# Kernel tuning notes

Hardware: AMD Instinct MI355X
Metric: run time of the kernel (lower is better)

Reference implementation:

```python
import jax, jax.numpy as jnp
import numpy as np


def _lstm_scan(x, w_ih, w_hh, b_ih, b_hh):
    """Unidirectional LSTM, PyTorch gate order (i, f, g, o).
    x: [B, T, C]; w_ih: [4H, C]; w_hh: [4H, H]. Returns [B, T, H]."""
    H = w_hh.shape[1]
    # Precompute input contribution for all timesteps (one big GEMM).
    xg = jnp.einsum('btc,gc->btg', x, w_ih) + b_ih + b_hh  # [B, T, 4H]

    def step(carry, xg_t):
        h, c = carry
        gates = xg_t + h @ w_hh.T
        i, f, g, o = jnp.split(gates, 4, axis=-1)
        c = jax.nn.sigmoid(f) * c + jax.nn.sigmoid(i) * jnp.tanh(g)
        h = jax.nn.sigmoid(o) * jnp.tanh(c)
        return (h, c), h

    B = x.shape[0]
    h0 = jnp.zeros((B, H), x.dtype)
    _, hs = jax.lax.scan(step, (h0, h0), jnp.swapaxes(xg, 0, 1))
    return jnp.swapaxes(hs, 0, 1)  # [B, T, H]


def _bilstm(x, w_ih_f, w_hh_f, b_ih_f, b_hh_f, w_ih_b, w_hh_b, b_ih_b, b_hh_b):
    fwd = _lstm_scan(x, w_ih_f, w_hh_f, b_ih_f, b_hh_f)
    bwd = _lstm_scan(x[:, ::-1], w_ih_b, w_hh_b, b_ih_b, b_hh_b)[:, ::-1]
    return jnp.concatenate([fwd, bwd], axis=-1)  # [B, T, 2H]


def setup_inputs() -> dict:
    key = jax.random.key(0)
    B, Hh, Ww, C, Hd = 64, 48, 48, 192, 48
    ks = jax.random.split(key, 20)
    s = 1.0 / np.sqrt(Hd)  # PyTorch LSTM init scale
    inp = {"x": jax.random.normal(ks[0], (B, Hh, Ww, C), jnp.float32)}
    names = ["v_w_ih_f", "v_w_hh_f", "v_b_ih_f", "v_b_hh_f",
             "v_w_ih_b", "v_w_hh_b", "v_b_ih_b", "v_b_hh_b",
             "h_w_ih_f", "h_w_hh_f", "h_b_ih_f", "h_b_hh_f",
             "h_w_ih_b", "h_w_hh_b", "h_b_ih_b", "h_b_hh_b"]
    shapes = [(4 * Hd, C), (4 * Hd, Hd), (4 * Hd,), (4 * Hd,)] * 4
    for i, (n, sh) in enumerate(zip(names, shapes)):
        inp[n] = jax.random.uniform(ks[1 + i], sh, jnp.float32, -s, s)
    inp["proj_w"] = jax.random.uniform(ks[17], (C, 4 * Hd), jnp.float32, -s, s)
    inp["proj_b"] = jax.random.uniform(ks[18], (C,), jnp.float32, -s, s)
    return inp


def reference(x, v_w_ih_f, v_w_hh_f, v_b_ih_f, v_b_hh_f,
              v_w_ih_b, v_w_hh_b, v_b_ih_b, v_b_hh_b,
              h_w_ih_f, h_w_hh_f, h_b_ih_f, h_b_hh_f,
              h_w_ih_b, h_w_hh_b, h_b_ih_b, h_b_hh_b,
              proj_w, proj_b):
    B, Hh, Ww, C = x.shape
    # Vertical: scan over height for each column.
    xv = jnp.transpose(x, (0, 2, 1, 3)).reshape(B * Ww, Hh, C)
    v = _bilstm(xv, v_w_ih_f, v_w_hh_f, v_b_ih_f, v_b_hh_f,
                v_w_ih_b, v_w_hh_b, v_b_ih_b, v_b_hh_b)
    v = jnp.transpose(v.reshape(B, Ww, Hh, -1), (0, 2, 1, 3))  # [B,H,W,2Hd]
    # Horizontal: scan over width for each row.
    xh = x.reshape(B * Hh, Ww, C)
    h = _bilstm(xh, h_w_ih_f, h_w_hh_f, h_b_ih_f, h_b_hh_f,
                h_w_ih_b, h_w_hh_b, h_b_ih_b, h_b_hh_b)
    h = h.reshape(B, Hh, Ww, -1)  # [B,H,W,2Hd]
    combined = jnp.concatenate([v, h], axis=-1)  # [B,H,W,4Hd]
    return jnp.einsum('bhwk,ck->bhwc', combined, proj_w) + proj_b
```

## Files before the change

kernel.cpp:

```cpp
#include <hip/hip_runtime.h>

typedef short short8 __attribute__((ext_vector_type(8)));
typedef short short4v __attribute__((ext_vector_type(4)));
typedef float f32x4 __attribute__((ext_vector_type(4)));
typedef unsigned short u16;

__device__ __forceinline__ u16 f2bf(float f) {
  unsigned int u = __builtin_bit_cast(unsigned int, f);
  u = (u + 0x7FFFu + ((u >> 16) & 1u)) >> 16;
  return (u16)u;
}
__device__ __forceinline__ short8 cvt8(float4 a, float4 b) {
  short8 v;
  v[0] = (short)f2bf(a.x); v[1] = (short)f2bf(a.y);
  v[2] = (short)f2bf(a.z); v[3] = (short)f2bf(a.w);
  v[4] = (short)f2bf(b.x); v[5] = (short)f2bf(b.y);
  v[6] = (short)f2bf(b.z); v[7] = (short)f2bf(b.w);
  return v;
}
__device__ __forceinline__ float sigmoidf_fast(float x) {
  return __builtin_amdgcn_rcpf(1.0f + __expf(-x));
}
__device__ __forceinline__ float tanhf_fast(float x) {
  return 1.0f - 2.0f * __builtin_amdgcn_rcpf(1.0f + __expf(2.0f * x));
}

#define NPX 147456

__global__ __launch_bounds__(256)
void xcvt_kernel(const float* __restrict__ x, u16* __restrict__ xbf)
{
  size_t c = ((size_t)blockIdx.x * 256 + threadIdx.x) * 8;
  const float4* p = (const float4*)(x + c);
  *(short8*)(xbf + c) = cvt8(p[0], p[1]);
}

__global__ __launch_bounds__(192)
void fused_scan_kernel(const u16* __restrict__ xbf,
    const float* __restrict__ wi0, const float* __restrict__ wi1,
    const float* __restrict__ wi2, const float* __restrict__ wi3,
    const float* __restrict__ u0, const float* __restrict__ u1,
    const float* __restrict__ u2, const float* __restrict__ u3,
    const float* __restrict__ bi0, const float* __restrict__ bh0,
    const float* __restrict__ bi1, const float* __restrict__ bh1,
    const float* __restrict__ bi2, const float* __restrict__ bh2,
    const float* __restrict__ bi3, const float* __restrict__ bh3,
    u16* __restrict__ comb)
{
  __shared__ u16 hl[2][1152];
  const int tid  = threadIdx.x;
  const int lane = tid & 63;
  const int wv   = tid >> 6;
  const int cl   = lane & 15;
  const int kg   = lane >> 4;
  const int W    = blockIdx.x;
  const int dir  = W / 192;
  const int g    = W - dir * 192;
  const int bb   = g / 3;
  const int rc   = (g - bb * 3) * 16 + cl;
  const bool vert = dir < 2;
  const bool bwd  = (dir & 1) != 0;

  const float* wp  = dir == 0 ? wi0 : dir == 1 ? wi1 : dir == 2 ? wi2 : wi3;
  const float* up  = dir == 0 ? u0  : dir == 1 ? u1  : dir == 2 ? u2  : u3;
  const float* bip = dir == 0 ? bi0 : dir == 1 ? bi1 : dir == 2 ? bi2 : bi3;
  const float* bhp = dir == 0 ? bh0 : dir == 1 ? bh1 : dir == 2 ? bh2 : bh3;

  const int tp0 = bwd ? 47 : 0;
  int px = vert ? (bb * 48 + tp0) * 48 + rc : (bb * 48 + rc) * 48 + tp0;
  const int dpx = (vert ? 48 : 1) * (bwd ? -1 : 1);

  short8 xfA[6], xfB[6];
  {
    const u16* xp = xbf + (size_t)px * 192 + kg * 8;
    #pragma unroll
    for (int kk = 0; kk < 6; ++kk) xfA[kk] = *(const short8*)(xp + kk * 32);
    const u16* xq = xbf + (size_t)(px + dpx) * 192 + kg * 8;
    #pragma unroll
    for (int kk = 0; kk < 6; ++kk) xfB[kk] = *(const short8*)(xq + kk * 32);
  }

  short8 wf[4][6];
  #pragma unroll
  for (int q = 0; q < 4; ++q) {
    int n = q * 48 + wv * 16 + cl;
    #pragma unroll
    for (int kk = 0; kk < 6; ++kk) {
      const float4* p = (const float4*)(wp + n * 192 + kk * 32 + kg * 8);
      wf[q][kk] = cvt8(p[0], p[1]);
    }
  }
  short8 uf[4][2];
  #pragma unroll
  for (int q = 0; q < 4; ++q) {
    int n = q * 48 + wv * 16 + cl;
    {
      const float4* p = (const float4*)(up + n * 48 + kg * 8);
      uf[q][0] = cvt8(p[0], p[1]);
    }
    if (kg < 2) {
      const float4* p = (const float4*)(up + n * 48 + 32 + kg * 8);
      uf[q][1] = cvt8(p[0], p[1]);
    } else {
      short8 z = {}; uf[q][1] = z;
    }
  }
  f32x4 bv[4];
  #pragma unroll
  for (int q = 0; q < 4; ++q)
    #pragma unroll
    for (int r = 0; r < 4; ++r) {
      int n = q * 48 + wv * 16 + kg * 4 + r;
      bv[q][r] = bip[n] + bhp[n];
    }

  u16* hz = &hl[0][0];
  for (int i = tid; i < 2304; i += 192) hz[i] = 0;
  __syncthreads();

  float c[4] = {0.f, 0.f, 0.f, 0.f};
  int cur = 0;
  u16* cb = comb + (size_t)dir * NPX * 48 + wv * 16 + kg * 4;

  const u16* xk = xbf + kg * 8;

  for (int it = 0; it < 24; ++it) {
    #pragma unroll
    for (int half = 0; half < 2; ++half) {
      short8* xf = half ? xfB : xfA;

      f32x4 acc[4];
      #pragma unroll
      for (int q = 0; q < 4; ++q) acc[q] = bv[q];
      #pragma unroll
      for (int kk = 0; kk < 6; ++kk)
        #pragma unroll
        for (int q = 0; q < 4; ++q)
          acc[q] = __builtin_amdgcn_mfma_f32_16x16x32_bf16(wf[q][kk], xf[kk], acc[q], 0, 0, 0);

      {
        int pp = px + 2 * dpx;
        pp = (pp < 0 || pp >= NPX) ? 0 : pp;
        const u16* xp = xk + (size_t)pp * 192;
        #pragma unroll
        for (int kk = 0; kk < 6; ++kk) xf[kk] = *(const short8*)(xp + kk * 32);
      }

      short8 hb0 = *(const short8*)&hl[cur][cl * 72 + kg * 8];
      short8 hb1 = *(const short8*)&hl[cur][cl * 72 + 32 + kg * 8];
      #pragma unroll
      for (int q = 0; q < 4; ++q)
        acc[q] = __builtin_amdgcn_mfma_f32_16x16x32_bf16(uf[q][0], hb0, acc[q], 0, 0, 0);
      #pragma unroll
      for (int q = 0; q < 4; ++q)
        acc[q] = __builtin_amdgcn_mfma_f32_16x16x32_bf16(uf[q][1], hb1, acc[q], 0, 0, 0);

      short4v h4;
      #pragma unroll
      for (int r = 0; r < 4; ++r) {
        float ii = sigmoidf_fast(acc[0][r]);
        float ff = sigmoidf_fast(acc[1][r]);
        float gg = tanhf_fast(acc[2][r]);
        float oo = sigmoidf_fast(acc[3][r]);
        float cc = ff * c[r] + ii * gg;
        c[r] = cc;
        h4[r] = (short)f2bf(oo * tanhf_fast(cc));
      }
      *(short4v*)&hl[cur ^ 1][cl * 72 + wv * 16 + kg * 4] = h4;
      *(short4v*)(cb + (size_t)px * 48) = h4;
      __syncthreads();
      cur ^= 1;
      px += dpx;
    }
  }
}

__global__ __launch_bounds__(256)
void proj_kernel(const u16* __restrict__ comb,
                 const float* __restrict__ pw,
                 const float* __restrict__ pb,
                 float* __restrict__ out)
{
  __shared__ u16 al[12288];
  const int tid  = threadIdx.x;
  const int lane = tid & 63;
  const int wv   = tid >> 6;
  const int cl   = lane & 15;
  const int kg   = lane >> 4;
  const int pxb  = blockIdx.x * 64;

  #pragma unroll
  for (int i = 0; i < 6; ++i) {
    int ch = tid + 256 * i;
    int pxl = ch / 24;
    int k0  = (ch % 24) << 3;
    int d   = k0 / 48;
    short8 v = *(const short8*)(comb + ((size_t)d * NPX + pxb + pxl) * 48 + (k0 - d * 48));
    *(short8*)&al[(pxl * 192 + k0) ^ ((pxl & 7) << 3)] = v;
  }

  short8 wf[3][6];
  #pragma unroll
  for (int nt = 0; nt < 3; ++nt) {
    int n = wv * 48 + nt * 16 + cl;
    #pragma unroll
    for (int kk = 0; kk < 6; ++kk) {
      const float4* p = (const float4*)(pw + n * 192 + kk * 32 + kg * 8);
      wf[nt][kk] = cvt8(p[0], p[1]);
    }
  }
  f32x4 bv[3];
  #pragma unroll
  for (int nt = 0; nt < 3; ++nt)
    #pragma unroll
    for (int r = 0; r < 4; ++r)
      bv[nt][r] = pb[wv * 48 + nt * 16 + kg * 4 + r];

  __syncthreads();

  f32x4 acc[3][4];
  #pragma unroll
  for (int nt = 0; nt < 3; ++nt)
    #pragma unroll
    for (int mi = 0; mi < 4; ++mi) acc[nt][mi] = bv[nt];

  #pragma unroll
  for (int kk = 0; kk < 6; ++kk) {
    short8 bfr[4];
    #pragma unroll
    for (int mi = 0; mi < 4; ++mi) {
      int row = mi * 16 + cl;
      bfr[mi] = *(const short8*)&al[(row * 192 + kk * 32 + kg * 8) ^ ((row & 7) << 3)];
    }
    #pragma unroll
    for (int nt = 0; nt < 3; ++nt)
      #pragma unroll
      for (int mi = 0; mi < 4; ++mi)
        acc[nt][mi] = __builtin_amdgcn_mfma_f32_16x16x32_bf16(wf[nt][kk], bfr[mi], acc[nt][mi], 0, 0, 0);
  }

  #pragma unroll
  for (int nt = 0; nt < 3; ++nt)
    #pragma unroll
    for (int mi = 0; mi < 4; ++mi) {
      size_t o = (size_t)(pxb + mi * 16 + cl) * 192 + wv * 48 + nt * 16 + kg * 4;
      *(f32x4*)(out + o) = acc[nt][mi];
    }
}

extern "C" void kernel_launch(void* const* d_in, const int* in_sizes, int n_in,
                              void* d_out, int out_size, void* d_ws, size_t ws_size,
                              hipStream_t stream) {
  const float* x = (const float*)d_in[0];
  u16* xbf  = (u16*)d_ws;
  u16* comb = (u16*)d_ws + (size_t)NPX * 192;

  xcvt_kernel<<<13824, 256, 0, stream>>>(x, xbf);

  fused_scan_kernel<<<768, 192, 0, stream>>>(
      xbf,
      (const float*)d_in[1], (const float*)d_in[5],
      (const float*)d_in[9], (const float*)d_in[13],
      (const float*)d_in[2], (const float*)d_in[6],
      (const float*)d_in[10], (const float*)d_in[14],
      (const float*)d_in[3],  (const float*)d_in[4],
      (const float*)d_in[7],  (const float*)d_in[8],
      (const float*)d_in[11], (const float*)d_in[12],
      (const float*)d_in[15], (const float*)d_in[16],
      comb);

  proj_kernel<<<2304, 256, 0, stream>>>(
      comb, (const float*)d_in[17], (const float*)d_in[18], (float*)d_out);
}
```

Measured before the change: 217.6 us.

## Split LSTM gate GEMMs across twice the waves and stage x through LDS

The scan kernel now launches 384 threads per block. Each wave pair splits the four gates: one wave computes i/f and the other g/o, and the g/o accumulators are exchanged through shared memory so that one wave applies the nonlinearities. The x tile for the next timestep is loaded cooperatively into a swizzled, double-buffered LDS buffer instead of per-lane register prefetch. The weights are prescaled by log2(e) so the activations can use exp2 directly. This halves the MFMA chain per wave on the serial critical path. In exchange it adds an extra barrier per step, LDS traffic, and half the waves sit idle during the activation phase.

```diff
diff --git a/kernel.cpp b/kernel.cpp
--- a/kernel.cpp
+++ b/kernel.cpp
@@ -18,14 +18,17 @@
   v[6] = (short)f2bf(b.z); v[7] = (short)f2bf(b.w);
   return v;
 }
-__device__ __forceinline__ float sigmoidf_fast(float x) {
-  return __builtin_amdgcn_rcpf(1.0f + __expf(-x));
-}
-__device__ __forceinline__ float tanhf_fast(float x) {
-  return 1.0f - 2.0f * __builtin_amdgcn_rcpf(1.0f + __expf(2.0f * x));
+__device__ __forceinline__ short8 cvt8s(float4 a, float4 b, float s) {
+  short8 v;
+  v[0] = (short)f2bf(a.x * s); v[1] = (short)f2bf(a.y * s);
+  v[2] = (short)f2bf(a.z * s); v[3] = (short)f2bf(a.w * s);
+  v[4] = (short)f2bf(b.x * s); v[5] = (short)f2bf(b.y * s);
+  v[6] = (short)f2bf(b.z * s); v[7] = (short)f2bf(b.w * s);
+  return v;
 }
 
 #define NPX 147456
+#define L2E 1.44269504088896f
 
 __global__ __launch_bounds__(256)
 void xcvt_kernel(const float* __restrict__ x, u16* __restrict__ xbf)
@@ -35,7 +38,7 @@
   *(short8*)(xbf + c) = cvt8(p[0], p[1]);
 }
 
-__global__ __launch_bounds__(192)
+__global__ __launch_bounds__(384)
 void fused_scan_kernel(const u16* __restrict__ xbf,
     const float* __restrict__ wi0, const float* __restrict__ wi1,
     const float* __restrict__ wi2, const float* __restrict__ wi3,
@@ -47,17 +50,23 @@
     const float* __restrict__ bi3, const float* __restrict__ bh3,
     u16* __restrict__ comb)
 {
+  __shared__ u16 xl[2][3072];
   __shared__ u16 hl[2][1152];
+  __shared__ f32x4 xga[3][64];
+  __shared__ f32x4 xgo[3][64];
+
   const int tid  = threadIdx.x;
   const int lane = tid & 63;
   const int wv   = tid >> 6;
+  const int s    = wv >> 1;
+  const int h    = wv & 1;
   const int cl   = lane & 15;
   const int kg   = lane >> 4;
   const int W    = blockIdx.x;
   const int dir  = W / 192;
   const int g    = W - dir * 192;
   const int bb   = g / 3;
-  const int rc   = (g - bb * 3) * 16 + cl;
+  const int rcb  = (g - bb * 3) * 16;
   const bool vert = dir < 2;
   const bool bwd  = (dir & 1) != 0;
 
@@ -67,111 +76,113 @@
   const float* bhp = dir == 0 ? bh0 : dir == 1 ? bh1 : dir == 2 ? bh2 : bh3;
 
   const int tp0 = bwd ? 47 : 0;
-  int px = vert ? (bb * 48 + tp0) * 48 + rc : (bb * 48 + rc) * 48 + tp0;
   const int dpx = (vert ? 48 : 1) * (bwd ? -1 : 1);
 
-  short8 xfA[6], xfB[6];
-  {
-    const u16* xp = xbf + (size_t)px * 192 + kg * 8;
-    #pragma unroll
-    for (int kk = 0; kk < 6; ++kk) xfA[kk] = *(const short8*)(xp + kk * 32);
-    const u16* xq = xbf + (size_t)(px + dpx) * 192 + kg * 8;
-    #pragma unroll
-    for (int kk = 0; kk < 6; ++kk) xfB[kk] = *(const short8*)(xq + kk * 32);
-  }
-
-  short8 wf[4][6];
-  #pragma unroll
-  for (int q = 0; q < 4; ++q) {
-    int n = q * 48 + wv * 16 + cl;
+  const int seq_l = tid / 24;
+  const int k0    = (tid % 24) * 8;
+  const int rc_t  = rcb + seq_l;
+  const int px_t0 = vert ? (bb * 48 + tp0) * 48 + rc_t
+                         : (bb * 48 + rc_t) * 48 + tp0;
+  const int swz_w = (seq_l * 192 + k0) ^ ((seq_l & 7) << 3);
+
+  short8 s0 = *(const short8*)(xbf + (size_t)px_t0 * 192 + k0);
+  *(short8*)&xl[0][swz_w] = s0;
+  const u16* xsrc = xbf + (size_t)(px_t0 + dpx) * 192 + k0;
+  const ptrdiff_t xstep = (ptrdiff_t)dpx * 192;
+
+  const int g0 = h ? 2 : 0;
+  const int g1 = h ? 3 : 1;
+  const float s0f = h ? 2.0f * L2E : L2E;
+  const float s1f = L2E;
+
+  short8 wf[2][6], uf[2][2];
+  f32x4 bv[2];
+  #pragma unroll
+  for (int j = 0; j < 2; ++j) {
+    int gj = j ? g1 : g0;
+    float sc = j ? s1f : s0f;
+    int n = gj * 48 + s * 16 + cl;
     #pragma unroll
     for (int kk = 0; kk < 6; ++kk) {
       const float4* p = (const float4*)(wp + n * 192 + kk * 32 + kg * 8);
-      wf[q][kk] = cvt8(p[0], p[1]);
-    }
-  }
-  short8 uf[4][2];
-  #pragma unroll
-  for (int q = 0; q < 4; ++q) {
-    int n = q * 48 + wv * 16 + cl;
+      wf[j][kk] = cvt8s(p[0], p[1], sc);
+    }
     {
       const float4* p = (const float4*)(up + n * 48 + kg * 8);
-      uf[q][0] = cvt8(p[0], p[1]);
+      uf[j][0] = cvt8s(p[0], p[1], sc);
     }
     if (kg < 2) {
       const float4* p = (const float4*)(up + n * 48 + 32 + kg * 8);
-      uf[q][1] = cvt8(p[0], p[1]);
+      uf[j][1] = cvt8s(p[0], p[1], sc);
     } else {
-      short8 z = {}; uf[q][1] = z;
-    }
-  }
-  f32x4 bv[4];
-  #pragma unroll
-  for (int q = 0; q < 4; ++q)
+      short8 z = {}; uf[j][1] = z;
+    }
     #pragma unroll
     for (int r = 0; r < 4; ++r) {
-      int n = q * 48 + wv * 16 + kg * 4 + r;
-      bv[q][r] = bip[n] + bhp[n];
-    }
-
-  u16* hz = &hl[0][0];
-  for (int i = tid; i < 2304; i += 192) hz[i] = 0;
+      int nb = gj * 48 + s * 16 + kg * 4 + r;
+      bv[j][r] = (bip[nb] + bhp[nb]) * sc;
+    }
+  }
+
+  for (int i = tid; i < 2304; i += 384) (&hl[0][0])[i] = 0;
   __syncthreads();
 
   float c[4] = {0.f, 0.f, 0.f, 0.f};
-  int cur = 0;
-  u16* cb = comb + (size_t)dir * NPX * 48 + wv * 16 + kg * 4;
-
-  const u16* xk = xbf + kg * 8;
-
-  for (int it = 0; it < 24; ++it) {
-    #pragma unroll
-    for (int half = 0; half < 2; ++half) {
-      short8* xf = half ? xfB : xfA;
-
-      f32x4 acc[4];
-      #pragma unroll
-      for (int q = 0; q < 4; ++q) acc[q] = bv[q];
-      #pragma unroll
-      for (int kk = 0; kk < 6; ++kk)
-        #pragma unroll
-        for (int q = 0; q < 4; ++q)
-          acc[q] = __builtin_amdgcn_mfma_f32_16x16x32_bf16(wf[q][kk], xf[kk], acc[q], 0, 0, 0);
-
-      {
-        int pp = px + 2 * dpx;
-        pp = (pp < 0 || pp >= NPX) ? 0 : pp;
-        const u16* xp = xk + (size_t)pp * 192;
-        #pragma unroll
-        for (int kk = 0; kk < 6; ++kk) xf[kk] = *(const short8*)(xp + kk * 32);
-      }
-
-      short8 hb0 = *(const short8*)&hl[cur][cl * 72 + kg * 8];
-      short8 hb1 = *(const short8*)&hl[cur][cl * 72 + 32 + kg * 8];
-      #pragma unroll
-      for (int q = 0; q < 4; ++q)
-        acc[q] = __builtin_amdgcn_mfma_f32_16x16x32_bf16(uf[q][0], hb0, acc[q], 0, 0, 0);
-      #pragma unroll
-      for (int q = 0; q < 4; ++q)
-        acc[q] = __builtin_amdgcn_mfma_f32_16x16x32_bf16(uf[q][1], hb1, acc[q], 0, 0, 0);
-
+  const int rc_l = rcb + cl;
+  const int px_l = vert ? (bb * 48 + tp0) * 48 + rc_l
+                        : (bb * 48 + rc_l) * 48 + tp0;
+  u16* cbp = comb + (size_t)dir * NPX * 48 + (size_t)px_l * 48 + s * 16 + kg * 4;
+  const ptrdiff_t cstep = (ptrdiff_t)dpx * 48;
+
+  int cur = 0, hcur = 0;
+
+  for (int t = 0; t < 48; ++t) {
+    short8 sa;
+    if (t < 47) { sa = *(const short8*)xsrc; xsrc += xstep; }
+
+    short8 xf[6];
+    #pragma unroll
+    for (int kk = 0; kk < 6; ++kk)
+      xf[kk] = *(const short8*)&xl[cur][(cl * 192 + kk * 32 + kg * 8) ^ ((cl & 7) << 3)];
+    short8 hb0 = *(const short8*)&hl[hcur][cl * 72 + kg * 8];
+    short8 hb1 = *(const short8*)&hl[hcur][cl * 72 + 32 + kg * 8];
+
+    f32x4 a0 = bv[0], a1 = bv[1];
+    #pragma unroll
+    for (int kk = 0; kk < 6; ++kk) {
+      a0 = __builtin_amdgcn_mfma_f32_16x16x32_bf16(wf[0][kk], xf[kk], a0, 0, 0, 0);
+      a1 = __builtin_amdgcn_mfma_f32_16x16x32_bf16(wf[1][kk], xf[kk], a1, 0, 0, 0);
+    }
+    a0 = __builtin_amdgcn_mfma_f32_16x16x32_bf16(uf[0][0], hb0, a0, 0, 0, 0);
+    a1 = __builtin_amdgcn_mfma_f32_16x16x32_bf16(uf[1][0], hb0, a1, 0, 0, 0);
+    a0 = __builtin_amdgcn_mfma_f32_16x16x32_bf16(uf[0][1], hb1, a0, 0, 0, 0);
+    a1 = __builtin_amdgcn_mfma_f32_16x16x32_bf16(uf[1][1], hb1, a1, 0, 0, 0);
+
+    if (h) { xga[s][lane] = a0; xgo[s][lane] = a1; }
+    __syncthreads();
+
+    if (!h) {
+      f32x4 aG = xga[s][lane];
+      f32x4 aO = xgo[s][lane];
       short4v h4;
       #pragma unroll
       for (int r = 0; r < 4; ++r) {
-        float ii = sigmoidf_fast(acc[0][r]);
-        float ff = sigmoidf_fast(acc[1][r]);
-        float gg = tanhf_fast(acc[2][r]);
-        float oo = sigmoidf_fast(acc[3][r]);
+        float ii = __builtin_amdgcn_rcpf(1.0f + __builtin_exp2f(-a0[r]));
+        float ff = __builtin_amdgcn_rcpf(1.0f + __builtin_exp2f(-a1[r]));
+        float gg = 1.0f - 2.0f * __builtin_amdgcn_rcpf(1.0f + __builtin_exp2f(aG[r]));
+        float oo = __builtin_amdgcn_rcpf(1.0f + __builtin_exp2f(-aO[r]));
         float cc = ff * c[r] + ii * gg;
         c[r] = cc;
-        h4[r] = (short)f2bf(oo * tanhf_fast(cc));
+        float th = 1.0f - 2.0f * __builtin_amdgcn_rcpf(1.0f + __builtin_exp2f(cc * (2.0f * L2E)));
+        h4[r] = (short)f2bf(oo * th);
       }
-      *(short4v*)&hl[cur ^ 1][cl * 72 + wv * 16 + kg * 4] = h4;
-      *(short4v*)(cb + (size_t)px * 48) = h4;
-      __syncthreads();
-      cur ^= 1;
-      px += dpx;
-    }
+      *(short4v*)&hl[hcur ^ 1][cl * 72 + s * 16 + kg * 4] = h4;
+      *(short4v*)cbp = h4;
+      cbp += cstep;
+    }
+    if (t < 47) *(short8*)&xl[cur ^ 1][swz_w] = sa;
+    __syncthreads();
+    cur ^= 1; hcur ^= 1;
   }
 }
 
@@ -193,10 +204,10 @@
   for (int i = 0; i < 6; ++i) {
     int ch = tid + 256 * i;
     int pxl = ch / 24;
-    int k0  = (ch % 24) << 3;
-    int d   = k0 / 48;
-    short8 v = *(const short8*)(comb + ((size_t)d * NPX + pxb + pxl) * 48 + (k0 - d * 48));
-    *(short8*)&al[(pxl * 192 + k0) ^ ((pxl & 7) << 3)] = v;
+    int kk0 = (ch % 24) << 3;
+    int d   = kk0 / 48;
+    short8 v = *(const short8*)(comb + ((size_t)d * NPX + pxb + pxl) * 48 + (kk0 - d * 48));
+    *(short8*)&al[(pxl * 192 + kk0) ^ ((pxl & 7) << 3)] = v;
   }
 
   short8 wf[3][6];
@@ -209,12 +220,12 @@
       wf[nt][kk] = cvt8(p[0], p[1]);
     }
   }
-  f32x4 bv[3];
+  f32x4 bvv[3];
   #pragma unroll
   for (int nt = 0; nt < 3; ++nt)
     #pragma unroll
     for (int r = 0; r < 4; ++r)
-      bv[nt][r] = pb[wv * 48 + nt * 16 + kg * 4 + r];
+      bvv[nt][r] = pb[wv * 48 + nt * 16 + kg * 4 + r];
 
   __syncthreads();
 
@@ -222,7 +233,7 @@
   #pragma unroll
   for (int nt = 0; nt < 3; ++nt)
     #pragma unroll
-    for (int mi = 0; mi < 4; ++mi) acc[nt][mi] = bv[nt];
+    for (int mi = 0; mi < 4; ++mi) acc[nt][mi] = bvv[nt];
 
   #pragma unroll
   for (int kk = 0; kk < 6; ++kk) {
@@ -257,7 +268,7 @@
 
   xcvt_kernel<<<13824, 256, 0, stream>>>(x, xbf);
 
-  fused_scan_kernel<<<768, 192, 0, stream>>>(
+  fused_scan_kernel<<<768, 384, 0, stream>>>(
       xbf,
       (const float*)d_in[1], (const float*)d_in[5],
       (const float*)d_in[9], (const float*)d_in[13],
```

After: 312.7 us. 43.7% more time.

## Software-pipeline input-projection MFMAs across steps and fold log2e into weights

Applied to the files above, without the earlier changes.

The scan loop now computes the next timestep's input-gate MFMAs (W_ih·x) before the current step's recurrent MFMAs, using ping-pong accumulators, so the x-dependent matrix work sits off the h-dependent critical path. Weights and biases are pre-scaled by log2(e) (twice that for the g gate), so the sigmoid and tanh can use exp2 directly without a multiply. The x prefetch becomes a single buffer advanced by pointer stride, with no bounds clamping. The trade-off is extra accumulator registers, plus a small rounding change because the scaling is applied before the bf16 conversion.

```diff
diff --git a/kernel.cpp b/kernel.cpp
--- a/kernel.cpp
+++ b/kernel.cpp
@@ -18,14 +18,17 @@
   v[6] = (short)f2bf(b.z); v[7] = (short)f2bf(b.w);
   return v;
 }
-__device__ __forceinline__ float sigmoidf_fast(float x) {
-  return __builtin_amdgcn_rcpf(1.0f + __expf(-x));
-}
-__device__ __forceinline__ float tanhf_fast(float x) {
-  return 1.0f - 2.0f * __builtin_amdgcn_rcpf(1.0f + __expf(2.0f * x));
+__device__ __forceinline__ short8 cvt8s(float4 a, float4 b, float s) {
+  short8 v;
+  v[0] = (short)f2bf(a.x * s); v[1] = (short)f2bf(a.y * s);
+  v[2] = (short)f2bf(a.z * s); v[3] = (short)f2bf(a.w * s);
+  v[4] = (short)f2bf(b.x * s); v[5] = (short)f2bf(b.y * s);
+  v[6] = (short)f2bf(b.z * s); v[7] = (short)f2bf(b.w * s);
+  return v;
 }
 
 #define NPX 147456
+#define L2E 1.44269504088896f
 
 __global__ __launch_bounds__(256)
 void xcvt_kernel(const float* __restrict__ x, u16* __restrict__ xbf)
@@ -67,111 +70,112 @@
   const float* bhp = dir == 0 ? bh0 : dir == 1 ? bh1 : dir == 2 ? bh2 : bh3;
 
   const int tp0 = bwd ? 47 : 0;
-  int px = vert ? (bb * 48 + tp0) * 48 + rc : (bb * 48 + rc) * 48 + tp0;
   const int dpx = (vert ? 48 : 1) * (bwd ? -1 : 1);
-
-  short8 xfA[6], xfB[6];
-  {
-    const u16* xp = xbf + (size_t)px * 192 + kg * 8;
-    #pragma unroll
-    for (int kk = 0; kk < 6; ++kk) xfA[kk] = *(const short8*)(xp + kk * 32);
-    const u16* xq = xbf + (size_t)(px + dpx) * 192 + kg * 8;
-    #pragma unroll
-    for (int kk = 0; kk < 6; ++kk) xfB[kk] = *(const short8*)(xq + kk * 32);
-  }
-
-  short8 wf[4][6];
+  const int px0 = vert ? (bb * 48 + tp0) * 48 + rc : (bb * 48 + rc) * 48 + tp0;
+
+  const u16* xp = xbf + (size_t)px0 * 192 + kg * 8;
+  const ptrdiff_t xstep = (ptrdiff_t)dpx * 192;
+
+  short8 xf[6];
+  #pragma unroll
+  for (int kk = 0; kk < 6; ++kk) xf[kk] = *(const short8*)(xp + kk * 32);
+
+  short8 wf[4][6], uf[4][2];
+  f32x4 bv[4];
   #pragma unroll
   for (int q = 0; q < 4; ++q) {
+    const float sc = (q == 2) ? 2.0f * L2E : L2E;
     int n = q * 48 + wv * 16 + cl;
     #pragma unroll
     for (int kk = 0; kk < 6; ++kk) {
       const float4* p = (const float4*)(wp + n * 192 + kk * 32 + kg * 8);
-      wf[q][kk] = cvt8(p[0], p[1]);
-    }
-  }
-  short8 uf[4][2];
-  #pragma unroll
-  for (int q = 0; q < 4; ++q) {
-    int n = q * 48 + wv * 16 + cl;
+      wf[q][kk] = cvt8s(p[0], p[1], sc);
+    }
     {
       const float4* p = (const float4*)(up + n * 48 + kg * 8);
-      uf[q][0] = cvt8(p[0], p[1]);
+      uf[q][0] = cvt8s(p[0], p[1], sc);
     }
     if (kg < 2) {
       const float4* p = (const float4*)(up + n * 48 + 32 + kg * 8);
-      uf[q][1] = cvt8(p[0], p[1]);
+      uf[q][1] = cvt8s(p[0], p[1], sc);
     } else {
       short8 z = {}; uf[q][1] = z;
     }
-  }
-  f32x4 bv[4];
-  #pragma unroll
-  for (int q = 0; q < 4; ++q)
     #pragma unroll
     for (int r = 0; r < 4; ++r) {
-      int n = q * 48 + wv * 16 + kg * 4 + r;
-      bv[q][r] = bip[n] + bhp[n];
-    }
-
-  u16* hz = &hl[0][0];
-  for (int i = tid; i < 2304; i += 192) hz[i] = 0;
+      int nb = q * 48 + wv * 16 + kg * 4 + r;
+      bv[q][r] = (bip[nb] + bhp[nb]) * sc;
+    }
+  }
+
+  for (int i = tid; i < 2304; i += 192) (&hl[0][0])[i] = 0;
   __syncthreads();
 
+  f32x4 pA[4], pB[4];
+  #pragma unroll
+  for (int q = 0; q < 4; ++q) pA[q] = bv[q];
+  #pragma unroll
+  for (int kk = 0; kk < 6; ++kk)
+    #pragma unroll
+    for (int q = 0; q < 4; ++q)
+      pA[q] = __builtin_amdgcn_mfma_f32_16x16x32_bf16(wf[q][kk], xf[kk], pA[q], 0, 0, 0);
+  xp += xstep;
+  #pragma unroll
+  for (int kk = 0; kk < 6; ++kk) xf[kk] = *(const short8*)(xp + kk * 32);
+
   float c[4] = {0.f, 0.f, 0.f, 0.f};
-  int cur = 0;
-  u16* cb = comb + (size_t)dir * NPX * 48 + wv * 16 + kg * 4;
-
-  const u16* xk = xbf + kg * 8;
-
-  for (int it = 0; it < 24; ++it) {
-    #pragma unroll
-    for (int half = 0; half < 2; ++half) {
-      short8* xf = half ? xfB : xfA;
-
-      f32x4 acc[4];
+  int hcur = 0;
+  u16* cbp = comb + (size_t)dir * NPX * 48 + (size_t)px0 * 48 + wv * 16 + kg * 4;
+  const ptrdiff_t cstep = (ptrdiff_t)dpx * 48;
+
+  auto STEP = [&](f32x4 (&cur)[4], f32x4 (&nxt)[4], int t) {
+    short8 hb0 = *(const short8*)&hl[hcur][cl * 72 + kg * 8];
+    short8 hb1 = *(const short8*)&hl[hcur][cl * 72 + 32 + kg * 8];
+
+    if (t < 47) {
       #pragma unroll
-      for (int q = 0; q < 4; ++q) acc[q] = bv[q];
+      for (int q = 0; q < 4; ++q) nxt[q] = bv[q];
       #pragma unroll
       for (int kk = 0; kk < 6; ++kk)
         #pragma unroll
         for (int q = 0; q < 4; ++q)
-          acc[q] = __builtin_amdgcn_mfma_f32_16x16x32_bf16(wf[q][kk], xf[kk], acc[q], 0, 0, 0);
-
-      {
-        int pp = px + 2 * dpx;
-        pp = (pp < 0 || pp >= NPX) ? 0 : pp;
-        const u16* xp = xk + (size_t)pp * 192;
+          nxt[q] = __builtin_amdgcn_mfma_f32_16x16x32_bf16(wf[q][kk], xf[kk], nxt[q], 0, 0, 0);
+      if (t < 46) {
+        xp += xstep;
         #pragma unroll
         for (int kk = 0; kk < 6; ++kk) xf[kk] = *(const short8*)(xp + kk * 32);
       }
-
-      short8 hb0 = *(const short8*)&hl[cur][cl * 72 + kg * 8];
-      short8 hb1 = *(const short8*)&hl[cur][cl * 72 + 32 + kg * 8];
-      #pragma unroll
-      for (int q = 0; q < 4; ++q)
-        acc[q] = __builtin_amdgcn_mfma_f32_16x16x32_bf16(uf[q][0], hb0, acc[q], 0, 0, 0);
-      #pragma unroll
-      for (int q = 0; q < 4; ++q)
-        acc[q] = __builtin_amdgcn_mfma_f32_16x16x32_bf16(uf[q][1], hb1, acc[q], 0, 0, 0);
-
-      short4v h4;
-      #pragma unroll
-      for (int r = 0; r < 4; ++r) {
-        float ii = sigmoidf_fast(acc[0][r]);
-        float ff = sigmoidf_fast(acc[1][r]);
-        float gg = tanhf_fast(acc[2][r]);
-        float oo = sigmoidf_fast(acc[3][r]);
-        float cc = ff * c[r] + ii * gg;
-        c[r] = cc;
-        h4[r] = (short)f2bf(oo * tanhf_fast(cc));
-      }
-      *(short4v*)&hl[cur ^ 1][cl * 72 + wv * 16 + kg * 4] = h4;
-      *(short4v*)(cb + (size_t)px * 48) = h4;
-      __syncthreads();
-      cur ^= 1;
-      px += dpx;
-    }
+    }
+
+    #pragma unroll
+    for (int q = 0; q < 4; ++q)
+      cur[q] = __builtin_amdgcn_mfma_f32_16x16x32_bf16(uf[q][0], hb0, cur[q], 0, 0, 0);
+    #pragma unroll
+    for (int q = 0; q < 4; ++q)
+      cur[q] = __builtin_amdgcn_mfma_f32_16x16x32_bf16(uf[q][1], hb1, cur[q], 0, 0, 0);
+
+    short4v h4;
+    #pragma unroll
+    for (int r = 0; r < 4; ++r) {
+      float ii = __builtin_amdgcn_rcpf(1.0f + __builtin_exp2f(-cur[0][r]));
+      float ff = __builtin_amdgcn_rcpf(1.0f + __builtin_exp2f(-cur[1][r]));
+      float gg = 1.0f - 2.0f * __builtin_amdgcn_rcpf(1.0f + __builtin_exp2f(cur[2][r]));
+      float oo = __builtin_amdgcn_rcpf(1.0f + __builtin_exp2f(-cur[3][r]));
+      float cc = ff * c[r] + ii * gg;
+      c[r] = cc;
+      float th = 1.0f - 2.0f * __builtin_amdgcn_rcpf(1.0f + __builtin_exp2f(cc * (2.0f * L2E)));
+      h4[r] = (short)f2bf(oo * th);
+    }
+    *(short4v*)&hl[hcur ^ 1][cl * 72 + wv * 16 + kg * 4] = h4;
+    *(short4v*)cbp = h4;
+    cbp += cstep;
+    __syncthreads();
+    hcur ^= 1;
+  };
+
+  for (int it = 0; it < 24; ++it) {
+    STEP(pA, pB, 2 * it);
+    STEP(pB, pA, 2 * it + 1);
   }
 }
 
@@ -193,10 +197,10 @@
   for (int i = 0; i < 6; ++i) {
     int ch = tid + 256 * i;
     int pxl = ch / 24;
-    int k0  = (ch % 24) << 3;
-    int d   = k0 / 48;
-    short8 v = *(const short8*)(comb + ((size_t)d * NPX + pxb + pxl) * 48 + (k0 - d * 48));
-    *(short8*)&al[(pxl * 192 + k0) ^ ((pxl & 7) << 3)] = v;
+    int kk0 = (ch % 24) << 3;
+    int d   = kk0 / 48;
+    short8 v = *(const short8*)(comb + ((size_t)d * NPX + pxb + pxl) * 48 + (kk0 - d * 48));
+    *(short8*)&al[(pxl * 192 + kk0) ^ ((pxl & 7) << 3)] = v;
   }
 
   short8 wf[3][6];
@@ -209,12 +213,12 @@
       wf[nt][kk] = cvt8(p[0], p[1]);
     }
   }
-  f32x4 bv[3];
+  f32x4 bvv[3];
   #pragma unroll
   for (int nt = 0; nt < 3; ++nt)
     #pragma unroll
     for (int r = 0; r < 4; ++r)
-      bv[nt][r] = pb[wv * 48 + nt * 16 + kg * 4 + r];
+      bvv[nt][r] = pb[wv * 48 + nt * 16 + kg * 4 + r];
 
   __syncthreads();
 
@@ -222,7 +226,7 @@
   #pragma unroll
   for (int nt = 0; nt < 3; ++nt)
     #pragma unroll
-    for (int mi = 0; mi < 4; ++mi) acc[nt][mi] = bv[nt];
+    for (int mi = 0; mi < 4; ++mi) acc[nt][mi] = bvv[nt];
 
   #pragma unroll
   for (int kk = 0; kk < 6; ++kk) {
```

New measurement: 228.8 us. +5.1%, slower.
